# Performance work log

Hardware: AMD Instinct MI355X
Metric: run time of the kernel (lower is better)

## Reference

```python
import jax, jax.numpy as jnp
import numpy as np

N = 100000
E = 3200000
IN_DIM = 256
OUT_DIM = 256
BN_EPS = 1e-5


def setup_inputs() -> dict:
    key = jax.random.key(0)
    k1, k2, k3, k4, k5 = jax.random.split(key, 5)
    x = jax.random.normal(k1, (N, IN_DIM), dtype=jnp.float32)
    edge_rows = jax.random.randint(k2, (E,), 0, N, dtype=jnp.int32)
    edge_cols = jax.random.randint(k3, (E,), 0, N, dtype=jnp.int32)
    edge_vals = jax.random.uniform(k4, (E,), dtype=jnp.float32)
    # xavier_uniform-like init for weight
    limit = float(np.sqrt(6.0 / (IN_DIM + OUT_DIM)))
    weight = jax.random.uniform(k5, (IN_DIM, OUT_DIM), minval=-limit, maxval=limit, dtype=jnp.float32)
    gamma = jnp.ones((OUT_DIM,), dtype=jnp.float32)
    beta = jnp.zeros((OUT_DIM,), dtype=jnp.float32)
    return {"x": x, "edge_rows": edge_rows, "edge_cols": edge_cols,
            "edge_vals": edge_vals, "weight": weight, "gamma": gamma, "beta": beta}


def reference(x, edge_rows, edge_cols, edge_vals, weight, gamma, beta):
    # dense projection: [N, in] @ [in, out] -> [N, out]
    z = jnp.matmul(x, weight)
    # sparse adjacency matmul (spmm): gather source rows, scale, scatter-add to dest
    msgs = edge_vals[:, None] * z[edge_cols]          # [E, out]
    agg = jax.ops.segment_sum(msgs, edge_rows, num_segments=N)  # [N, out]
    # BatchNorm1d (training mode: batch stats, biased variance) + ReLU
    mean = jnp.mean(agg, axis=0)
    var = jnp.mean(jnp.square(agg - mean), axis=0)
    norm = (agg - mean) * jax.lax.rsqrt(var + BN_EPS) * gamma + beta
    return jax.nn.relu(norm)
```

## Files before the change

kernel.cpp:

```cpp
#include <hip/hip_runtime.h>
#include <hip/hip_bf16.h>

#define N_NODES 100000
#define N_EDGES 3200000
#define DIM 256
#define BN_EPS 1e-5f
#define BROWS 256
#define NBUCK ((N_NODES + BROWS - 1) / BROWS)
#define BIN_BLOCKS 512
#define EPB (N_EDGES / BIN_BLOCKS)
#define RPW 4
#define NPART 64
#define CAP 10240

typedef __attribute__((ext_vector_type(8))) short short8v;
typedef __attribute__((ext_vector_type(4))) float f32x4;

__device__ __forceinline__ float b2f(unsigned short h) {
    return __uint_as_float(((unsigned int)h) << 16);
}
__device__ __forceinline__ unsigned short f2b(float f) {
    unsigned int u = __float_as_uint(f);
    unsigned int rounded = u + 0x7FFF + ((u >> 16) & 1);
    return (unsigned short)(rounded >> 16);
}

__global__ __launch_bounds__(256) void wfrag_kernel(const float* __restrict__ W,
                                                    unsigned short* __restrict__ wfrag) {
    const int t = blockIdx.x * 256 + threadIdx.x;
    const int e = t & 7;
    const int l = (t >> 3) & 63;
    const int frag = t >> 9;
    const int nt = frag >> 3;
    const int ks = frag & 7;
    const int k = ks * 32 + ((l >> 4) << 3) + e;
    const int c = nt * 16 + (l & 15);
    wfrag[t] = f2b(W[k * DIM + c]);
}

__global__ __launch_bounds__(256) void gemm_mfma_kernel(const float* __restrict__ x,
                                                        const unsigned short* __restrict__ wfrag,
                                                        unsigned short* __restrict__ zb) {
    const int wid = (blockIdx.x * blockDim.x + threadIdx.x) >> 6;
    const int lane = threadIdx.x & 63;
    if (wid >= N_NODES / 16) return;
    const int m0 = wid * 16;

    const int arow = m0 + (lane & 15);
    const int kb = (lane >> 4) << 3;
    const float* xrow = x + (size_t)arow * DIM + kb;
    short8v af[8];
    #pragma unroll
    for (int ks = 0; ks < 8; ++ks) {
        const float4 a0 = *(const float4*)(xrow + ks * 32);
        const float4 a1 = *(const float4*)(xrow + ks * 32 + 4);
        short8v f;
        f[0] = (short)f2b(a0.x); f[1] = (short)f2b(a0.y);
        f[2] = (short)f2b(a0.z); f[3] = (short)f2b(a0.w);
        f[4] = (short)f2b(a1.x); f[5] = (short)f2b(a1.y);
        f[6] = (short)f2b(a1.z); f[7] = (short)f2b(a1.w);
        af[ks] = f;
    }

    const int drow0 = m0 + ((lane >> 4) << 2);
    const int dcol = lane & 15;
    for (int nt = 0; nt < 16; ++nt) {
        f32x4 acc = {0.f, 0.f, 0.f, 0.f};
        const unsigned short* wp = wfrag + ((size_t)(nt * 8) * 64 + lane) * 8;
        #pragma unroll
        for (int ks = 0; ks < 8; ++ks) {
            const short8v bf = *(const short8v*)(wp + (size_t)ks * 64 * 8);
            acc = __builtin_amdgcn_mfma_f32_16x16x32_bf16(af[ks], bf, acc, 0, 0, 0);
        }
        unsigned short* zp = zb + (size_t)drow0 * DIM + nt * 16 + dcol;
        zp[0]       = f2b(acc[0]);
        zp[DIM]     = f2b(acc[1]);
        zp[2 * DIM] = f2b(acc[2]);
        zp[3 * DIM] = f2b(acc[3]);
    }
}

__global__ __launch_bounds__(256) void bin_kernel(const int* __restrict__ rows,
                                                  const int* __restrict__ cols,
                                                  const float* __restrict__ vals,
                                                  int* bucketCnt,
                                                  int2* __restrict__ gBinned) {
    __shared__ int h[NBUCK];
    __shared__ int base[NBUCK];
    __shared__ int cur[NBUCK];
    const int t = threadIdx.x;
    const int e0 = blockIdx.x * EPB;
    for (int i = t; i < NBUCK; i += 256) h[i] = 0;
    __syncthreads();
    for (int e = e0 + t; e < e0 + EPB; e += 256)
        atomicAdd(&h[rows[e] >> 8], 1);
    __syncthreads();
    for (int b = t; b < NBUCK; b += 256) {
        cur[b] = 0;
        if (h[b]) base[b] = atomicAdd(&bucketCnt[b], h[b]);
    }
    __syncthreads();
    for (int e = e0 + t; e < e0 + EPB; e += 256) {
        const int r = rows[e];
        const int b = r >> 8;
        const int rk = atomicAdd(&cur[b], 1);
        int2 p;
        p.x = ((r & 255) << 17) | cols[e];
        p.y = __float_as_int(vals[e]);
        gBinned[(size_t)b * CAP + base[b] + rk] = p;
    }
}

__global__ __launch_bounds__(256) void fine_sort_kernel(const int* __restrict__ bucketCnt,
                                                        const int2* __restrict__ gBinned,
                                                        int* __restrict__ row_ptr,
                                                        int* __restrict__ row_end,
                                                        int2* __restrict__ finalE) {
    __shared__ int h[BROWS];
    __shared__ int s[BROWS];
    __shared__ int cur[BROWS];
    const int t = threadIdx.x;
    const int b = blockIdx.x;
    const int base0 = b * CAP;
    const int cnt = bucketCnt[b];
    h[t] = 0;
    __syncthreads();
    for (int e = base0 + t; e < base0 + cnt; e += 256)
        atomicAdd(&h[gBinned[e].x >> 17], 1);
    __syncthreads();
    s[t] = h[t];
    __syncthreads();
    for (int off = 1; off < BROWS; off <<= 1) {
        int x = (t >= off) ? s[t - off] : 0;
        __syncthreads();
        s[t] += x;
        __syncthreads();
    }
    const int excl = s[t] - h[t];
    const int grow = b * BROWS + t;
    if (grow < N_NODES) {
        row_ptr[grow] = base0 + excl;
        row_end[grow] = base0 + s[t];
    }
    cur[t] = excl;
    __syncthreads();
    for (int e = base0 + t; e < base0 + cnt; e += 256) {
        const int2 p = gBinned[e];
        const int rl = p.x >> 17;
        const int rk = atomicAdd(&cur[rl], 1);
        int2 q;
        q.x = p.x & 0x1FFFF;
        q.y = p.y;
        finalE[base0 + rk] = q;
    }
}

__global__ __launch_bounds__(256) void spmm_csr_kernel(const int* __restrict__ row_ptr,
                                                       const int* __restrict__ row_end,
                                                       const int2* __restrict__ pairs,
                                                       const unsigned short* __restrict__ zb,
                                                       float* __restrict__ out,
                                                       float* __restrict__ partials) {
    __shared__ float sdata[2 * DIM];
    const int t = threadIdx.x;
    sdata[t] = 0.f;
    sdata[t + 256] = 0.f;
    __syncthreads();

    const int wave = (blockIdx.x * 256 + t) >> 6;
    const int lane = t & 63;
    const int row0 = wave * RPW;

    float4 s  = make_float4(0.f, 0.f, 0.f, 0.f);
    float4 sq = make_float4(0.f, 0.f, 0.f, 0.f);

    for (int row = row0; row < row0 + RPW; ++row) {
        const int start = __builtin_amdgcn_readfirstlane(row_ptr[row]);
        const int end   = __builtin_amdgcn_readfirstlane(row_end[row]);
        float4 acc = make_float4(0.f, 0.f, 0.f, 0.f);
        int2 pA[8], pB[8];
        ushort4 mA[8], mB[8];

#define LOADX(P, M, EB) do { \
    _Pragma("unroll") for (int j = 0; j < 8; ++j) P[j] = pairs[(EB) + j]; \
    _Pragma("unroll") for (int j = 0; j < 8; ++j) \
        M[j] = ((const ushort4*)(zb + (size_t)P[j].x * DIM))[lane]; \
  } while (0)
#define FMAX(P, M) do { \
    _Pragma("unroll") for (int j = 0; j < 8; ++j) { \
        const float v = __int_as_float(P[j].y); \
        acc.x += v * b2f(M[j].x); \
        acc.y += v * b2f(M[j].y); \
        acc.z += v * b2f(M[j].z); \
        acc.w += v * b2f(M[j].w); \
    } \
  } while (0)

        const int nb = (end - start) >> 3;
        int e = start;
        if (nb) {
            LOADX(pA, mA, e); e += 8;
            int b = 1;
            for (; b + 1 < nb; b += 2) {
                LOADX(pB, mB, e); e += 8;
                FMAX(pA, mA);
                LOADX(pA, mA, e); e += 8;
                FMAX(pB, mB);
            }
            if (b < nb) {
                LOADX(pB, mB, e); e += 8;
                FMAX(pA, mA);
                FMAX(pB, mB);
            } else {
                FMAX(pA, mA);
            }
        }
        const int rem = end - e;
        if (rem) {
            #pragma unroll
            for (int j = 0; j < 8; ++j) if (j < rem) pA[j] = pairs[e + j];
            #pragma unroll
            for (int j = 0; j < 8; ++j) if (j < rem)
                mA[j] = ((const ushort4*)(zb + (size_t)pA[j].x * DIM))[lane];
            #pragma unroll
            for (int j = 0; j < 8; ++j) if (j < rem) {
                const float v = __int_as_float(pA[j].y);
                acc.x += v * b2f(mA[j].x);
                acc.y += v * b2f(mA[j].y);
                acc.z += v * b2f(mA[j].z);
                acc.w += v * b2f(mA[j].w);
            }
        }
#undef LOADX
#undef FMAX

        f32x4 st = {acc.x, acc.y, acc.z, acc.w};
        __builtin_nontemporal_store(st, (f32x4*)(out + (size_t)row * DIM) + lane);

        s.x += acc.x; s.y += acc.y; s.z += acc.z; s.w += acc.w;
        sq.x += acc.x * acc.x; sq.y += acc.y * acc.y;
        sq.z += acc.z * acc.z; sq.w += acc.w * acc.w;
    }

    const int c0 = lane * 4;
    atomicAdd(&sdata[c0 + 0], s.x);
    atomicAdd(&sdata[c0 + 1], s.y);
    atomicAdd(&sdata[c0 + 2], s.z);
    atomicAdd(&sdata[c0 + 3], s.w);
    atomicAdd(&sdata[256 + c0 + 0], sq.x);
    atomicAdd(&sdata[256 + c0 + 1], sq.y);
    atomicAdd(&sdata[256 + c0 + 2], sq.z);
    atomicAdd(&sdata[256 + c0 + 3], sq.w);
    __syncthreads();

    float* pb = partials + (size_t)(blockIdx.x & (NPART - 1)) * (2 * DIM);
    atomicAdd(&pb[t], sdata[t]);
    atomicAdd(&pb[t + 256], sdata[t + 256]);
}

__global__ __launch_bounds__(256) void finalize_kernel(const float* __restrict__ partials,
                                                       const float* __restrict__ gamma,
                                                       const float* __restrict__ beta,
                                                       float* __restrict__ sb) {
    const int c = threadIdx.x;
    float s = 0.f, ssq = 0.f;
    for (int b = 0; b < NPART; ++b) {
        s   += partials[b * (2 * DIM) + c];
        ssq += partials[b * (2 * DIM) + 256 + c];
    }
    const float inv_n = 1.0f / (float)N_NODES;
    const float mean = s * inv_n;
    float var = ssq * inv_n - mean * mean;
    const float rstd = rsqrtf(var + BN_EPS);
    const float scale = rstd * gamma[c];
    sb[c] = scale;
    sb[DIM + c] = beta[c] - mean * scale;
}

#define NORM_BLOCKS 2048
__global__ __launch_bounds__(256) void norm_kernel(float* __restrict__ out,
                                                   const float* __restrict__ sb) {
    const int c0 = (threadIdx.x & 63) * 4;
    const float s0 = sb[c0 + 0], s1 = sb[c0 + 1], s2 = sb[c0 + 2], s3 = sb[c0 + 3];
    const float b0 = sb[DIM + c0 + 0], b1 = sb[DIM + c0 + 1];
    const float b2 = sb[DIM + c0 + 2], b3 = sb[DIM + c0 + 3];
    const int nvec = N_NODES * (DIM / 4);
    for (int idx = blockIdx.x * 256 + threadIdx.x; idx < nvec; idx += NORM_BLOCKS * 256) {
        float4 a = ((float4*)out)[idx];
        float4 o;
        o.x = fmaxf(fmaf(a.x, s0, b0), 0.f);
        o.y = fmaxf(fmaf(a.y, s1, b1), 0.f);
        o.z = fmaxf(fmaf(a.z, s2, b2), 0.f);
        o.w = fmaxf(fmaf(a.w, s3, b3), 0.f);
        ((float4*)out)[idx] = o;
    }
}

extern "C" void kernel_launch(void* const* d_in, const int* in_sizes, int n_in,
                              void* d_out, int out_size, void* d_ws, size_t ws_size,
                              hipStream_t stream) {
    const float* x         = (const float*)d_in[0];
    const int*   edge_rows = (const int*)d_in[1];
    const int*   edge_cols = (const int*)d_in[2];
    const float* edge_vals = (const float*)d_in[3];
    const float* weight    = (const float*)d_in[4];
    const float* gamma     = (const float*)d_in[5];
    const float* beta      = (const float*)d_in[6];
    float* out = (float*)d_out;

    unsigned short* zb    = (unsigned short*)d_ws;
    int2*  gBinned  = (int2*)d_ws;
    unsigned short* wfrag = zb + (size_t)N_NODES * DIM;
    int2*  finalE   = (int2*)(wfrag + DIM * DIM);
    int*   row_ptr  = (int*)(finalE + (size_t)NBUCK * CAP);
    int*   row_end  = row_ptr + N_NODES;
    int*   bucketCnt = row_end + N_NODES;
    float* partials = (float*)(bucketCnt + NBUCK);
    float* sb       = partials + NPART * 2 * DIM;

    hipMemsetAsync(bucketCnt, 0, (NBUCK + NPART * 2 * DIM) * sizeof(int), stream);

    bin_kernel<<<BIN_BLOCKS, 256, 0, stream>>>(edge_rows, edge_cols, edge_vals, bucketCnt, gBinned);
    fine_sort_kernel<<<NBUCK, 256, 0, stream>>>(bucketCnt, gBinned, row_ptr, row_end, finalE);

    wfrag_kernel<<<DIM * DIM / 256, 256, 0, stream>>>(weight, wfrag);
    gemm_mfma_kernel<<<(N_NODES / 16 + 3) / 4, 256, 0, stream>>>(x, wfrag, zb);

    spmm_csr_kernel<<<N_NODES / (RPW * 4), 256, 0, stream>>>(row_ptr, row_end, finalE, zb, out, partials);

    finalize_kernel<<<1, 256, 0, stream>>>(partials, gamma, beta, sb);
    norm_kernel<<<NORM_BLOCKS, 256, 0, stream>>>(out, sb);
}
```

Before: 454.2 us.

## Merge independent preprocessing stages into combined launches via block-index dispatch

Fuses the weight-fragment conversion into the edge binning kernel and the bf16 GEMM into the fine-sort kernel, using blockIdx ranges to select which job each block runs. This removes two launches and lets independent work overlap on the GPU instead of serialising. Because gBinned previously aliased the zb buffer, it now gets its own workspace region so the GEMM writes cannot clobber binned edges, which enlarges the workspace footprint. Mixing heterogeneous blocks in one launch may also change occupancy, since the shared-memory and register needs of each branch are combined.

```diff
diff --git a/kernel.cpp b/kernel.cpp
--- a/kernel.cpp
+++ b/kernel.cpp
@@ -12,6 +12,8 @@
 #define RPW 4
 #define NPART 64
 #define CAP 10240
+#define WFRAG_BLOCKS (DIM * DIM / 256)
+#define GEMM_BLOCKS ((N_NODES / 16 + 3) / 4)
 
 typedef __attribute__((ext_vector_type(8))) short short8v;
 typedef __attribute__((ext_vector_type(4))) float f32x4;
@@ -25,70 +27,31 @@
     return (unsigned short)(rounded >> 16);
 }
 
-__global__ __launch_bounds__(256) void wfrag_kernel(const float* __restrict__ W,
-                                                    unsigned short* __restrict__ wfrag) {
-    const int t = blockIdx.x * 256 + threadIdx.x;
-    const int e = t & 7;
-    const int l = (t >> 3) & 63;
-    const int frag = t >> 9;
-    const int nt = frag >> 3;
-    const int ks = frag & 7;
-    const int k = ks * 32 + ((l >> 4) << 3) + e;
-    const int c = nt * 16 + (l & 15);
-    wfrag[t] = f2b(W[k * DIM + c]);
-}
-
-__global__ __launch_bounds__(256) void gemm_mfma_kernel(const float* __restrict__ x,
-                                                        const unsigned short* __restrict__ wfrag,
-                                                        unsigned short* __restrict__ zb) {
-    const int wid = (blockIdx.x * blockDim.x + threadIdx.x) >> 6;
-    const int lane = threadIdx.x & 63;
-    if (wid >= N_NODES / 16) return;
-    const int m0 = wid * 16;
-
-    const int arow = m0 + (lane & 15);
-    const int kb = (lane >> 4) << 3;
-    const float* xrow = x + (size_t)arow * DIM + kb;
-    short8v af[8];
-    #pragma unroll
-    for (int ks = 0; ks < 8; ++ks) {
-        const float4 a0 = *(const float4*)(xrow + ks * 32);
-        const float4 a1 = *(const float4*)(xrow + ks * 32 + 4);
-        short8v f;
-        f[0] = (short)f2b(a0.x); f[1] = (short)f2b(a0.y);
-        f[2] = (short)f2b(a0.z); f[3] = (short)f2b(a0.w);
-        f[4] = (short)f2b(a1.x); f[5] = (short)f2b(a1.y);
-        f[6] = (short)f2b(a1.z); f[7] = (short)f2b(a1.w);
-        af[ks] = f;
-    }
-
-    const int drow0 = m0 + ((lane >> 4) << 2);
-    const int dcol = lane & 15;
-    for (int nt = 0; nt < 16; ++nt) {
-        f32x4 acc = {0.f, 0.f, 0.f, 0.f};
-        const unsigned short* wp = wfrag + ((size_t)(nt * 8) * 64 + lane) * 8;
-        #pragma unroll
-        for (int ks = 0; ks < 8; ++ks) {
-            const short8v bf = *(const short8v*)(wp + (size_t)ks * 64 * 8);
-            acc = __builtin_amdgcn_mfma_f32_16x16x32_bf16(af[ks], bf, acc, 0, 0, 0);
-        }
-        unsigned short* zp = zb + (size_t)drow0 * DIM + nt * 16 + dcol;
-        zp[0]       = f2b(acc[0]);
-        zp[DIM]     = f2b(acc[1]);
-        zp[2 * DIM] = f2b(acc[2]);
-        zp[3 * DIM] = f2b(acc[3]);
-    }
-}
-
-__global__ __launch_bounds__(256) void bin_kernel(const int* __restrict__ rows,
-                                                  const int* __restrict__ cols,
-                                                  const float* __restrict__ vals,
-                                                  int* bucketCnt,
-                                                  int2* __restrict__ gBinned) {
+__global__ __launch_bounds__(256) void bin_wfrag_kernel(const int* __restrict__ rows,
+                                                        const int* __restrict__ cols,
+                                                        const float* __restrict__ vals,
+                                                        int* bucketCnt,
+                                                        int2* __restrict__ gBinned,
+                                                        const float* __restrict__ W,
+                                                        unsigned short* __restrict__ wfrag) {
     __shared__ int h[NBUCK];
     __shared__ int base[NBUCK];
     __shared__ int cur[NBUCK];
     const int t = threadIdx.x;
+
+    if (blockIdx.x >= BIN_BLOCKS) {
+        const int g = (blockIdx.x - BIN_BLOCKS) * 256 + t;
+        const int e = g & 7;
+        const int l = (g >> 3) & 63;
+        const int frag = g >> 9;
+        const int nt = frag >> 3;
+        const int ks = frag & 7;
+        const int k = ks * 32 + ((l >> 4) << 3) + e;
+        const int c = nt * 16 + (l & 15);
+        wfrag[g] = f2b(W[k * DIM + c]);
+        return;
+    }
+
     const int e0 = blockIdx.x * EPB;
     for (int i = t; i < NBUCK; i += 256) h[i] = 0;
     __syncthreads();
@@ -111,15 +74,60 @@
     }
 }
 
-__global__ __launch_bounds__(256) void fine_sort_kernel(const int* __restrict__ bucketCnt,
+__global__ __launch_bounds__(256) void sort_gemm_kernel(const int* __restrict__ bucketCnt,
                                                         const int2* __restrict__ gBinned,
                                                         int* __restrict__ row_ptr,
                                                         int* __restrict__ row_end,
-                                                        int2* __restrict__ finalE) {
+                                                        int2* __restrict__ finalE,
+                                                        const float* __restrict__ x,
+                                                        const unsigned short* __restrict__ wfrag,
+                                                        unsigned short* __restrict__ zb) {
     __shared__ int h[BROWS];
     __shared__ int s[BROWS];
     __shared__ int cur[BROWS];
     const int t = threadIdx.x;
+
+    if (blockIdx.x >= NBUCK) {
+        const int wid = ((blockIdx.x - NBUCK) * 256 + t) >> 6;
+        const int lane = t & 63;
+        if (wid >= N_NODES / 16) return;
+        const int m0 = wid * 16;
+
+        const int arow = m0 + (lane & 15);
+        const int kb = (lane >> 4) << 3;
+        const float* xrow = x + (size_t)arow * DIM + kb;
+        short8v af[8];
+        #pragma unroll
+        for (int ks = 0; ks < 8; ++ks) {
+            const float4 a0 = *(const float4*)(xrow + ks * 32);
+            const float4 a1 = *(const float4*)(xrow + ks * 32 + 4);
+            short8v f;
+            f[0] = (short)f2b(a0.x); f[1] = (short)f2b(a0.y);
+            f[2] = (short)f2b(a0.z); f[3] = (short)f2b(a0.w);
+            f[4] = (short)f2b(a1.x); f[5] = (short)f2b(a1.y);
+            f[6] = (short)f2b(a1.z); f[7] = (short)f2b(a1.w);
+            af[ks] = f;
+        }
+
+        const int drow0 = m0 + ((lane >> 4) << 2);
+        const int dcol = lane & 15;
+        for (int nt = 0; nt < 16; ++nt) {
+            f32x4 acc = {0.f, 0.f, 0.f, 0.f};
+            const unsigned short* wp = wfrag + ((size_t)(nt * 8) * 64 + lane) * 8;
+            #pragma unroll
+            for (int ks = 0; ks < 8; ++ks) {
+                const short8v bf = *(const short8v*)(wp + (size_t)ks * 64 * 8);
+                acc = __builtin_amdgcn_mfma_f32_16x16x32_bf16(af[ks], bf, acc, 0, 0, 0);
+            }
+            unsigned short* zp = zb + (size_t)drow0 * DIM + nt * 16 + dcol;
+            zp[0]       = f2b(acc[0]);
+            zp[DIM]     = f2b(acc[1]);
+            zp[2 * DIM] = f2b(acc[2]);
+            zp[3 * DIM] = f2b(acc[3]);
+        }
+        return;
+    }
+
     const int b = blockIdx.x;
     const int base0 = b * CAP;
     const int cnt = bucketCnt[b];
@@ -131,9 +139,9 @@
     s[t] = h[t];
     __syncthreads();
     for (int off = 1; off < BROWS; off <<= 1) {
-        int x = (t >= off) ? s[t - off] : 0;
+        int x2 = (t >= off) ? s[t - off] : 0;
         __syncthreads();
-        s[t] += x;
+        s[t] += x2;
         __syncthreads();
     }
     const int excl = s[t] - h[t];
@@ -309,9 +317,9 @@
     float* out = (float*)d_out;
 
     unsigned short* zb    = (unsigned short*)d_ws;
-    int2*  gBinned  = (int2*)d_ws;
     unsigned short* wfrag = zb + (size_t)N_NODES * DIM;
-    int2*  finalE   = (int2*)(wfrag + DIM * DIM);
+    int2*  gBinned  = (int2*)(wfrag + DIM * DIM);
+    int2*  finalE   = gBinned + (size_t)NBUCK * CAP;
     int*   row_ptr  = (int*)(finalE + (size_t)NBUCK * CAP);
     int*   row_end  = row_ptr + N_NODES;
     int*   bucketCnt = row_end + N_NODES;
@@ -320,11 +328,11 @@
 
     hipMemsetAsync(bucketCnt, 0, (NBUCK + NPART * 2 * DIM) * sizeof(int), stream);
 
-    bin_kernel<<<BIN_BLOCKS, 256, 0, stream>>>(edge_rows, edge_cols, edge_vals, bucketCnt, gBinned);
-    fine_sort_kernel<<<NBUCK, 256, 0, stream>>>(bucketCnt, gBinned, row_ptr, row_end, finalE);
-
-    wfrag_kernel<<<DIM * DIM / 256, 256, 0, stream>>>(weight, wfrag);
-    gemm_mfma_kernel<<<(N_NODES / 16 + 3) / 4, 256, 0, stream>>>(x, wfrag, zb);
+    bin_wfrag_kernel<<<BIN_BLOCKS + WFRAG_BLOCKS, 256, 0, stream>>>(
+        edge_rows, edge_cols, edge_vals, bucketCnt, gBinned, weight, wfrag);
+
+    sort_gemm_kernel<<<NBUCK + GEMM_BLOCKS, 256, 0, stream>>>(
+        bucketCnt, gBinned, row_ptr, row_end, finalE, x, wfrag, zb);
 
     spmm_csr_kernel<<<N_NODES / (RPW * 4), 256, 0, stream>>>(row_ptr, row_end, finalE, zb, out, partials);
 
```

After: 436.5 us. 1.04x faster.
